# Kernel optimization log

Measured on AMD Instinct MI355X. Metric: run time of the kernel, lower is better.

Reference implementation:

```python
import jax, jax.numpy as jnp
import numpy as np

B = 512        # batch
P = 32 * 6 * 6 # 1152 primary capsules
C = 10         # digit capsules (n_caps)
D = 16         # output capsule dim (n_dims)
IN = 8         # primary capsule dim
ITERS = 3      # routing iterations


def setup_inputs() -> dict:
    key = jax.random.key(0)
    k1, k2 = jax.random.split(key)
    x = jax.random.normal(k1, (B, P, IN), dtype=jnp.float32)
    # routing_weights param (leading batch-1 dim squeezed; broadcast replaces repeat)
    W = jax.random.normal(k2, (P, C, D, IN), dtype=jnp.float32)
    return {"x": x, "W": W}


def squash(t, axis=-1, eps=1e-7):
    sq = jnp.sum(t * t, axis=axis, keepdims=True)
    return (sq / (1.0 + sq)) * t / jnp.sqrt(sq + eps)


def reference(x, W):
    # prediction vectors u_hat: [B, P, C, D]  (equiv to W@x with repeats replaced by einsum)
    u_hat = jnp.einsum('pcdi,bpi->bpcd', W, x)
    logits = jnp.zeros((B, P, C), dtype=x.dtype)
    v = None
    for i in range(ITERS):
        coup = jax.nn.softmax(logits, axis=2)                  # over n_caps, matches dim=2
        s = jnp.einsum('bpc,bpcd->bcd', coup, u_hat)           # sum over primary caps (dim=1)
        v = squash(s, axis=-1)                                 # squash over capsule dim (torch dim=-2)
        if i != ITERS - 1:
            agreement = jnp.einsum('bpcd,bcd->bpc', u_hat, v)  # u_hat^T @ v
            logits = logits + agreement
    # match torch output shape [B, 1, C, D, 1]
    return v[:, None, :, :, None]
```

## Files before the change

kernel.cpp:

```cpp
#include <hip/hip_runtime.h>
#include <hip/hip_bf16.h>

#define NB 512
#define NP 1152
#define NC 10
#define ND 16
#define NI 8

constexpr int K_B    = 2;
constexpr int B_TILE = 4 * 4 * K_B;
constexpr int P_TILE = 8;
constexpr int NBLK_B = NB / B_TILE;
constexpr int NBLK_P = NP / P_TILE;
constexpr int SVD = NB * NC * ND;
constexpr int W_TILE_BYTES = P_TILE * NC * ND * NI * 4;
constexpr int X_TILE_FLOATS = B_TILE * P_TILE * NI;

constexpr float LOG2E = 1.4426950408889634f;

typedef float v2f __attribute__((ext_vector_type(2)));

__device__ __forceinline__ float red16_dpp(float v) {
    int t;
    t = __builtin_amdgcn_update_dpp(0, __float_as_int(v), 0xB1, 0xF, 0xF, true);
    v += __int_as_float(t);
    t = __builtin_amdgcn_update_dpp(0, __float_as_int(v), 0x4E, 0xF, 0xF, true);
    v += __int_as_float(t);
    t = __builtin_amdgcn_update_dpp(0, __float_as_int(v), 0x124, 0xF, 0xF, true);
    v += __int_as_float(t);
    t = __builtin_amdgcn_update_dpp(0, __float_as_int(v), 0x128, 0xF, 0xF, true);
    v += __int_as_float(t);
    return v;
}

template<int PASS>
__global__ __launch_bounds__(256, 2)
void caps_pass(const float* __restrict__ x,
               const float* __restrict__ w,
               const float* __restrict__ v0,
               const float* __restrict__ v1,
               float* __restrict__ s_out)
{
    __shared__ __align__(16) float w_lds[W_TILE_BYTES / 4];
    __shared__ __align__(16) float x_lds[X_TILE_FLOATS];

    const int tid  = threadIdx.x;
    const int lane = tid & 63;
    const int wave = tid >> 6;
    const int d    = lane & 15;
    const int bsub = lane >> 4;
    const int bblk = blockIdx.x % NBLK_B;
    const int pblk = blockIdx.x / NBLK_B;
    const int p0   = pblk * P_TILE;

    {
        const uint8_t* wsrc = (const uint8_t*)w + (size_t)pblk * W_TILE_BYTES;
        const int lane_src = (lane << 4) ^ ((lane & 8) << 1) ^ ((lane & 16) << 1);
        #pragma unroll
        for (int j = 0; j < 10; ++j) {
            const int off = wave * 10240 + j * 1024;
            __builtin_amdgcn_global_load_lds(
                (const __attribute__((address_space(1))) void*)(wsrc + off + lane_src),
                (__attribute__((address_space(3))) void*)((uint8_t*)w_lds + off),
                16, 0, 0);
        }
    }

    {
        #pragma unroll
        for (int j = 0; j < 2; ++j) {
            const int u   = wave * 128 + j * 64 + lane;
            const int bl  = u >> 4;
            const int w16 = u & 15;
            const float* bbase = x + ((size_t)(bblk * B_TILE + bl) * NP + p0) * NI;
            const uint8_t* src = (const uint8_t*)bbase + ((w16 ^ (bl & 3)) * 16);
            __builtin_amdgcn_global_load_lds(
                (const __attribute__((address_space(1))) void*)src,
                (__attribute__((address_space(3))) void*)((uint8_t*)x_lds + (size_t)u * 16),
                16, 0, 0);
        }
    }

    int bidx[K_B];
    #pragma unroll
    for (int k = 0; k < K_B; ++k) bidx[k] = bblk * B_TILE + wave * 8 + k * 4 + bsub;

    float vr[K_B][NC];
    if (PASS >= 1) {
        #pragma unroll
        for (int k = 0; k < K_B; ++k)
            #pragma unroll
            for (int c = 0; c < NC; ++c) {
                float vv = v0[(bidx[k] * NC + c) * ND + d];
                if (PASS == 2) vv += v1[(bidx[k] * NC + c) * ND + d];
                vr[k][c] = vv * LOG2E;
            }
    }

    float sacc[K_B][NC];
    #pragma unroll
    for (int k = 0; k < K_B; ++k)
        #pragma unroll
        for (int c = 0; c < NC; ++c) sacc[k][c] = 0.0f;

    const int lane_rd = (d << 5) ^ ((d & 4) << 2) ^ ((d & 8) << 2);
    const int xswz    = bsub << 4;

    asm volatile("s_waitcnt vmcnt(0)" ::: "memory");
    __syncthreads();

    for (int pp = 0; pp < P_TILE; ++pp) {
        v2f xv[K_B][4];
        #pragma unroll
        for (int k = 0; k < K_B; ++k) {
            const int xb = ((wave * 8 + k * 4 + bsub) * 256 + pp * 32) ^ xswz;
            const uint8_t* xp = (const uint8_t*)x_lds;
            const float4 a = *(const float4*)(xp + xb);
            const float4 b = *(const float4*)(xp + (xb ^ 16));
            xv[k][0] = v2f{a.x, a.y};
            xv[k][1] = v2f{a.z, a.w};
            xv[k][2] = v2f{b.x, b.y};
            xv[k][3] = v2f{b.z, b.w};
        }

        float uh[K_B][NC];
        #pragma unroll
        for (int c = 0; c < NC; ++c) {
            const uint8_t* pb = (const uint8_t*)w_lds + pp * 5120 + c * 512;
            const float4 wa = *(const float4*)(pb + lane_rd);
            const float4 wb = *(const float4*)(pb + (lane_rd ^ 16));
            const v2f w01{wa.x, wa.y}, w23{wa.z, wa.w};
            const v2f w45{wb.x, wb.y}, w67{wb.z, wb.w};
            #pragma unroll
            for (int k = 0; k < K_B; ++k) {
                v2f acc = w01 * xv[k][0];
                acc = __builtin_elementwise_fma(w23, xv[k][1], acc);
                acc = __builtin_elementwise_fma(w45, xv[k][2], acc);
                acc = __builtin_elementwise_fma(w67, xv[k][3], acc);
                const float u = acc[0] + acc[1];
                if (PASS == 0) sacc[k][c] = fmaf(0.1f, u, sacc[k][c]);
                else           uh[k][c] = u;
            }
        }

        if (PASS >= 1) {
            #pragma unroll
            for (int k = 0; k < K_B; ++k) {
                float lg[NC];
                #pragma unroll
                for (int c = 0; c < NC; ++c)
                    lg[c] = red16_dpp(uh[k][c] * vr[k][c]);
                float ssum = 0.0f;
                float coup[NC];
                #pragma unroll
                for (int c = 0; c < NC; ++c) {
                    coup[c] = __builtin_amdgcn_exp2f(lg[c]);
                    ssum += coup[c];
                }
                const float inv = __builtin_amdgcn_rcpf(ssum);
                #pragma unroll
                for (int c = 0; c < NC; ++c)
                    sacc[k][c] = fmaf(coup[c] * inv, uh[k][c], sacc[k][c]);
            }
        }
    }

    #pragma unroll
    for (int k = 0; k < K_B; ++k)
        #pragma unroll
        for (int c = 0; c < NC; ++c)
            atomicAdd(&s_out[(bidx[k] * NC + c) * ND + d], sacc[k][c]);
}

template<bool ZERO_S>
__global__ __launch_bounds__(256)
void caps_squash(float* __restrict__ s, float* __restrict__ v)
{
    const int idx = blockIdx.x * 256 + threadIdx.x;
    const float sv = s[idx];
    if (ZERO_S) s[idx] = 0.0f;
    float sq = red16_dpp(sv * sv);
    const float scale = (sq / (1.0f + sq)) / sqrtf(sq + 1e-7f);
    v[idx] = scale * sv;
}

extern "C" void kernel_launch(void* const* d_in, const int* in_sizes, int n_in,
                              void* d_out, int out_size, void* d_ws, size_t ws_size,
                              hipStream_t stream)
{
    const float* x = (const float*)d_in[0];
    const float* w = (const float*)d_in[1];
    float* out = (float*)d_out;

    float* s  = (float*)d_ws;
    float* v0 = s + SVD;
    float* v1 = out;

    const dim3 pgrid(NBLK_B * NBLK_P);
    const dim3 pblock(256);
    const dim3 qgrid(SVD / 256);
    const dim3 qblock(256);

    hipMemsetAsync(s, 0, (size_t)SVD * sizeof(float), stream);
    caps_pass<0><<<pgrid, pblock, 0, stream>>>(x, w, nullptr, nullptr, s);
    caps_squash<true><<<qgrid, qblock, 0, stream>>>(s, v0);
    caps_pass<1><<<pgrid, pblock, 0, stream>>>(x, w, v0, nullptr, s);
    caps_squash<true><<<qgrid, qblock, 0, stream>>>(s, v1);
    caps_pass<2><<<pgrid, pblock, 0, stream>>>(x, w, v0, v1, s);
    caps_squash<false><<<qgrid, qblock, 0, stream>>>(s, out);
}
```

Baseline: 180.8 us.

## Replace global atomics with per-block partial buffers and a reduce-squash kernel

Each pass kernel now writes its per-P-tile partial sums to a private slice of a large workspace instead of doing atomicAdd into one shared s buffer. A new kernel then sums the 144 partial slices per element and applies squash. This removes atomic contention and the memset. The cost is a workspace of about 46 MB that is written and read back on every routing iteration. The new path runs only if ws_size is large enough; otherwise the old atomic path is used.

```diff
diff --git a/kernel.cpp b/kernel.cpp
--- a/kernel.cpp
+++ b/kernel.cpp
@@ -33,7 +33,7 @@
     return v;
 }
 
-template<int PASS>
+template<int PASS, bool TS>
 __global__ __launch_bounds__(256, 2)
 void caps_pass(const float* __restrict__ x,
                const float* __restrict__ w,
@@ -165,11 +165,42 @@
         }
     }
 
+    if (TS) {
+        float* pout = s_out + (size_t)pblk * SVD;
+        #pragma unroll
+        for (int k = 0; k < K_B; ++k)
+            #pragma unroll
+            for (int c = 0; c < NC; ++c)
+                pout[(bidx[k] * NC + c) * ND + d] = sacc[k][c];
+    } else {
+        #pragma unroll
+        for (int k = 0; k < K_B; ++k)
+            #pragma unroll
+            for (int c = 0; c < NC; ++c)
+                atomicAdd(&s_out[(bidx[k] * NC + c) * ND + d], sacc[k][c]);
+    }
+}
+
+__global__ __launch_bounds__(256)
+void caps_reduce_squash(const float* __restrict__ part, float* __restrict__ v)
+{
+    const int idx = blockIdx.x * 256 + threadIdx.x;
+    float a0 = 0, a1 = 0, a2 = 0, a3 = 0, a4 = 0, a5 = 0, a6 = 0, a7 = 0;
     #pragma unroll
-    for (int k = 0; k < K_B; ++k)
-        #pragma unroll
-        for (int c = 0; c < NC; ++c)
-            atomicAdd(&s_out[(bidx[k] * NC + c) * ND + d], sacc[k][c]);
+    for (int r = 0; r < NBLK_P; r += 8) {
+        a0 += part[(size_t)(r + 0) * SVD + idx];
+        a1 += part[(size_t)(r + 1) * SVD + idx];
+        a2 += part[(size_t)(r + 2) * SVD + idx];
+        a3 += part[(size_t)(r + 3) * SVD + idx];
+        a4 += part[(size_t)(r + 4) * SVD + idx];
+        a5 += part[(size_t)(r + 5) * SVD + idx];
+        a6 += part[(size_t)(r + 6) * SVD + idx];
+        a7 += part[(size_t)(r + 7) * SVD + idx];
+    }
+    const float sv = ((a0 + a1) + (a2 + a3)) + ((a4 + a5) + (a6 + a7));
+    float sq = red16_dpp(sv * sv);
+    const float scale = (sq / (1.0f + sq)) / sqrtf(sq + 1e-7f);
+    v[idx] = scale * sv;
 }
 
 template<bool ZERO_S>
@@ -192,20 +223,35 @@
     const float* w = (const float*)d_in[1];
     float* out = (float*)d_out;
 
-    float* s  = (float*)d_ws;
-    float* v0 = s + SVD;
-    float* v1 = out;
-
     const dim3 pgrid(NBLK_B * NBLK_P);
     const dim3 pblock(256);
     const dim3 qgrid(SVD / 256);
     const dim3 qblock(256);
 
-    hipMemsetAsync(s, 0, (size_t)SVD * sizeof(float), stream);
-    caps_pass<0><<<pgrid, pblock, 0, stream>>>(x, w, nullptr, nullptr, s);
-    caps_squash<true><<<qgrid, qblock, 0, stream>>>(s, v0);
-    caps_pass<1><<<pgrid, pblock, 0, stream>>>(x, w, v0, nullptr, s);
-    caps_squash<true><<<qgrid, qblock, 0, stream>>>(s, v1);
-    caps_pass<2><<<pgrid, pblock, 0, stream>>>(x, w, v0, v1, s);
-    caps_squash<false><<<qgrid, qblock, 0, stream>>>(s, out);
-}
+    const size_t partBytes = (size_t)NBLK_P * SVD * sizeof(float);
+
+    if (ws_size >= partBytes + (size_t)SVD * sizeof(float)) {
+        float* part = (float*)d_ws;
+        float* v0   = (float*)((uint8_t*)d_ws + partBytes);
+        float* v1   = out;
+
+        caps_pass<0, true><<<pgrid, pblock, 0, stream>>>(x, w, nullptr, nullptr, part);
+        caps_reduce_squash<<<qgrid, qblock, 0, stream>>>(part, v0);
+        caps_pass<1, true><<<pgrid, pblock, 0, stream>>>(x, w, v0, nullptr, part);
+        caps_reduce_squash<<<qgrid, qblock, 0, stream>>>(part, v1);
+        caps_pass<2, true><<<pgrid, pblock, 0, stream>>>(x, w, v0, v1, part);
+        caps_reduce_squash<<<qgrid, qblock, 0, stream>>>(part, out);
+    } else {
+        float* s  = (float*)d_ws;
+        float* v0 = s + SVD;
+        float* v1 = out;
+
+        hipMemsetAsync(s, 0, (size_t)SVD * sizeof(float), stream);
+        caps_pass<0, false><<<pgrid, pblock, 0, stream>>>(x, w, nullptr, nullptr, s);
+        caps_squash<true><<<qgrid, qblock, 0, stream>>>(s, v0);
+        caps_pass<1, false><<<pgrid, pblock, 0, stream>>>(x, w, v0, nullptr, s);
+        caps_squash<true><<<qgrid, qblock, 0, stream>>>(s, v1);
+        caps_pass<2, false><<<pgrid, pblock, 0, stream>>>(x, w, v0, v1, s);
+        caps_squash<false><<<qgrid, qblock, 0, stream>>>(s, out);
+    }
+}
```

Measured after the change: 182.4 us. No clear change (+0.9%).
